# Kernel tuning notes

Hardware: AMD Instinct MI355X
Metric: run time of the kernel (lower is better)

Reference implementation:

```python
import jax, jax.numpy as jnp
import numpy as np

N = 16_777_216  # total nodes
B = 16_384      # graphs per batch


def setup_inputs() -> dict:
    key = jax.random.key(0)
    ks = jax.random.split(key, 9)
    x = jax.random.normal(ks[0], (N, 1), dtype=jnp.float32)
    batch = jnp.sort(jax.random.randint(ks[1], (N,), 0, B)).astype(jnp.int64)
    node_type = jax.random.randint(ks[2], (N,), 0, 3).astype(jnp.int64)
    # MLP params (torch Linear default-ish init scale)
    W1 = jax.random.normal(ks[3], (4, 32), dtype=jnp.float32) * 0.5
    b1 = jax.random.normal(ks[4], (32,), dtype=jnp.float32) * 0.1
    W2 = jax.random.normal(ks[5], (32, 16), dtype=jnp.float32) * 0.18
    b2 = jax.random.normal(ks[6], (16,), dtype=jnp.float32) * 0.1
    W3 = jax.random.normal(ks[7], (16, 1), dtype=jnp.float32) * 0.25
    b3 = jax.random.normal(ks[8], (1,), dtype=jnp.float32) * 0.1
    return {"x": x, "batch": batch, "node_type": node_type, "num_graphs": B,
            "W1": W1, "b1": b1, "W2": W2, "b2": b2, "W3": W3, "b3": b3}


def reference(x, batch, node_type, num_graphs, W1, b1, W2, b2, W3, b3):
    # Per-graph node-type histogram: one fused segment pass over (N, 4)
    # columns = [count(nt==0), count(nt==1), count(nt==2), total_nodes]
    onehot = jax.nn.one_hot(node_type, 3, dtype=jnp.float32)           # (N, 3)
    per_node = jnp.concatenate([onehot, jnp.ones((onehot.shape[0], 1), jnp.float32)], axis=1)  # (N, 4)
    feats = jax.ops.segment_sum(per_node, batch, num_segments=num_graphs)  # (B, 4)
    feats = feats - jnp.array([54.5, 0.0, 0.0, 56.5], dtype=jnp.float32)
    h = jax.nn.relu(feats @ W1 + b1)
    h = jax.nn.relu(h @ W2 + b2)
    return h @ W3 + b3  # (B, 1)
```

## Files before the change

kernel.cpp:

```cpp
#include <hip/hip_runtime.h>


constexpr int GPW = 4;

__device__ __forceinline__ int interp_lower_bound(
    const int* __restrict__ batch, int n, int stride, int g)
{
    int blo = 0, bhi = n;
    long long pos = (long long)g * stride - (stride >> 1);
    int it = 0;
    while (bhi - blo > 4) {
        int p;
        if (it < 5) {
            long long pc = pos;
            if (pc < blo) pc = blo;
            if (pc > bhi - 4) pc = bhi - 4;
            p = (int)pc & ~3;
            ++it;
        } else {
            p = ((blo + bhi) >> 1) & ~3;
            if (p > bhi - 4) p = bhi - 4;
        }
        const int4 q = *(const int4*)(batch + p);
        if (q.w < g) {
            blo = p + 4;
            pos = p + 4 + (long long)(g - q.w) * stride - (stride >> 1);
        } else if (q.x >= g) {
            bhi = p;
            pos = p + (long long)(g - q.x) * stride - (stride >> 1);
        } else {
            return p + 1 + (q.y < g) + (q.z < g);
        }
    }
    if (bhi > blo) {
        const int4 q = *(const int4*)(batch + blo);
        return blo + (q.x < g) + (q.y < g) + (q.z < g) + (q.w < g);
    }
    return blo;
}

__global__ __launch_bounds__(256) void fused_kernel(
    const int* __restrict__ batch, const int* __restrict__ ntype,
    const float* __restrict__ W1, const float* __restrict__ b1,
    const float* __restrict__ W2, const float* __restrict__ b2,
    const float* __restrict__ W3, const float* __restrict__ b3,
    float* __restrict__ out, int n, int B, int stride)
{
    __shared__ float sW1[128], sW2[512], sb1[32], sb2[16], sW3[16], sb3v[1];
    const int tid = threadIdx.x;
    if (tid < 128) sW1[tid] = W1[tid];
    sW2[tid]       = W2[tid];
    sW2[tid + 256] = W2[tid + 256];
    if      (tid < 32)  sb1[tid]      = b1[tid];
    else if (tid < 48)  sb2[tid - 32] = b2[tid - 32];
    else if (tid < 64)  sW3[tid - 48] = W3[tid - 48];
    else if (tid == 64) sb3v[0]       = b3[0];
    __syncthreads();

    const int wid  = (blockIdx.x * 256 + tid) >> 6;
    const int lane = tid & 63;
    const int g0   = wid * GPW;
    if (g0 >= B) return;

    int ans = 0;
    if (lane <= GPW) {
        const int g = min(g0 + lane, B);
        ans = interp_lower_bound(batch, n, stride, g);
    }

    for (int i = 0; i < GPW; ++i) {
        const int g = g0 + i;
        if (g >= B) break;
        const int s   = __shfl(ans, i);
        const int e   = __shfl(ans, i + 1);
        const int len = e - s;

        int c0 = 0, c1 = 0;
        int sa = (s + 3) & ~3; if (sa > e) sa = e;
        int ea = e & ~3;       if (ea < sa) ea = sa;

        {
            const int idx = s + lane;
            if (idx < sa) { const int v = ntype[idx]; c0 += (v == 0); c1 += (v == 1); }
        }
        {
            const int4* nt4 = (const int4*)ntype;
            for (int q = (sa >> 2) + lane; q < (ea >> 2); q += 64) {
                const int4 v = nt4[q];
                c0 += (v.x == 0) + (v.y == 0) + (v.z == 0) + (v.w == 0);
                c1 += (v.x == 1) + (v.y == 1) + (v.z == 1) + (v.w == 1);
            }
        }
        {
            const int idx = ea + lane;
            if (idx < e) { const int v = ntype[idx]; c0 += (v == 0); c1 += (v == 1); }
        }

        unsigned long long p = (unsigned)c0 | ((unsigned long long)(unsigned)c1 << 32);
        #pragma unroll
        for (int off = 32; off; off >>= 1) p += __shfl_xor(p, off);
        const int c0t = (int)(p & 0xFFFFFFFFull);
        const int c1t = (int)(p >> 32);

        const float f0 = (float)c0t - 54.5f;
        const float f1 = (float)c1t;
        const float f2 = (float)(len - c0t - c1t);
        const float f3 = (float)len - 56.5f;

        const int j = lane & 31;
        float h1 = sb1[j];
        h1 = fmaf(f0, sW1[      j], h1);
        h1 = fmaf(f1, sW1[ 32 + j], h1);
        h1 = fmaf(f2, sW1[ 64 + j], h1);
        h1 = fmaf(f3, sW1[ 96 + j], h1);
        h1 = fmaxf(0.0f, h1);

        const int m = lane & 15;
        float s2 = sb2[m];
        #pragma unroll
        for (int jj = 0; jj < 32; ++jj)
            s2 = fmaf(__shfl(h1, jj), sW2[jj * 16 + m], s2);
        const float h2 = fmaxf(0.0f, s2);

        float p3 = h2 * sW3[m];
        p3 += __shfl_xor(p3, 8);
        p3 += __shfl_xor(p3, 4);
        p3 += __shfl_xor(p3, 2);
        p3 += __shfl_xor(p3, 1);

        if (lane == 0) out[g] = p3 + sb3v[0];
    }
}

extern "C" void kernel_launch(void* const* d_in, const int* in_sizes, int n_in,
                              void* d_out, int out_size, void* d_ws, size_t ws_size,
                              hipStream_t stream) {
    const int*   batch = (const int*)d_in[1];
    const int*   ntype = (const int*)d_in[2];
    const float* W1    = (const float*)d_in[4];
    const float* b1    = (const float*)d_in[5];
    const float* W2    = (const float*)d_in[6];
    const float* b2    = (const float*)d_in[7];
    const float* W3    = (const float*)d_in[8];
    const float* b3    = (const float*)d_in[9];
    float*       out   = (float*)d_out;

    const int n = in_sizes[1];
    const int B = out_size;

    const int waves  = (B + GPW - 1) / GPW;
    const int blocks = (waves * 64 + 255) / 256;
    fused_kernel<<<blocks, 256, 0, stream>>>(
        batch, ntype, W1, b1, W2, b2, W3, b3, out, n, B, n / B);
}
```

Baseline: 28.96 us.

## Process two graphs per wave with unrolled clamped loads and split MLP halves

Each wave now handles two graphs instead of four, which doubles the wave count. The streaming loop over node types is unrolled five times with clamped unconditional loads so that many independent 16-byte loads are in flight before the predicated accumulation. The two graphs' reductions are interleaved, and the MLP runs once with each half-wave evaluating one graph, instead of running serially per graph. This targets memory latency and serial per-graph overhead, at the cost of more binary searches overall and some wasted loads on short segments.

```diff
diff --git a/kernel.cpp b/kernel.cpp
--- a/kernel.cpp
+++ b/kernel.cpp
@@ -1,7 +1,8 @@
 #include <hip/hip_runtime.h>
 
 
-constexpr int GPW = 4;
+constexpr int GPW = 2;
+constexpr int UNR = 5;
 
 __device__ __forceinline__ int interp_lower_bound(
     const int* __restrict__ batch, int n, int stride, int g)
@@ -63,73 +64,90 @@
     if (g0 >= B) return;
 
     int ans = 0;
-    if (lane <= GPW) {
-        const int g = min(g0 + lane, B);
-        ans = interp_lower_bound(batch, n, stride, g);
-    }
+    if (lane <= GPW) ans = interp_lower_bound(batch, n, stride, min(g0 + lane, B));
+    const int s0 = __shfl(ans, 0);
+    const int s1 = __shfl(ans, 1);
+    const int s2b = __shfl(ans, 2);
 
-    for (int i = 0; i < GPW; ++i) {
-        const int g = g0 + i;
-        if (g >= B) break;
-        const int s   = __shfl(ans, i);
-        const int e   = __shfl(ans, i + 1);
-        const int len = e - s;
+    const int4* nt4 = (const int4*)ntype;
+    const int nqm1 = (n >> 2) - 1;
+    int c0[2] = {0, 0}, c1[2] = {0, 0};
 
-        int c0 = 0, c1 = 0;
+    #pragma unroll
+    for (int i = 0; i < 2; ++i) {
+        const int s = (i == 0) ? s0 : s1;
+        const int e = (i == 0) ? s1 : s2b;
         int sa = (s + 3) & ~3; if (sa > e) sa = e;
         int ea = e & ~3;       if (ea < sa) ea = sa;
 
         {
             const int idx = s + lane;
-            if (idx < sa) { const int v = ntype[idx]; c0 += (v == 0); c1 += (v == 1); }
+            if (idx < sa) { const int v = ntype[idx]; c0[i] += (v == 0); c1[i] += (v == 1); }
         }
-        {
-            const int4* nt4 = (const int4*)ntype;
-            for (int q = (sa >> 2) + lane; q < (ea >> 2); q += 64) {
-                const int4 v = nt4[q];
-                c0 += (v.x == 0) + (v.y == 0) + (v.z == 0) + (v.w == 0);
-                c1 += (v.x == 1) + (v.y == 1) + (v.z == 1) + (v.w == 1);
+        const int qa = (sa >> 2) + lane;
+        const int qe = (ea >> 2);
+        #pragma unroll
+        for (int u = 0; u < UNR; ++u) {
+            const int qi = qa + u * 64;
+            const int4 v = nt4[min(qi, nqm1)];
+            if (qi < qe) {
+                c0[i] += (v.x == 0) + (v.y == 0) + (v.z == 0) + (v.w == 0);
+                c1[i] += (v.x == 1) + (v.y == 1) + (v.z == 1) + (v.w == 1);
             }
+        }
+        for (int qi = qa + UNR * 64; qi < qe; qi += 64) {
+            const int4 v = nt4[qi];
+            c0[i] += (v.x == 0) + (v.y == 0) + (v.z == 0) + (v.w == 0);
+            c1[i] += (v.x == 1) + (v.y == 1) + (v.z == 1) + (v.w == 1);
         }
         {
             const int idx = ea + lane;
-            if (idx < e) { const int v = ntype[idx]; c0 += (v == 0); c1 += (v == 1); }
+            if (idx < e) { const int v = ntype[idx]; c0[i] += (v == 0); c1[i] += (v == 1); }
         }
+    }
 
-        unsigned long long p = (unsigned)c0 | ((unsigned long long)(unsigned)c1 << 32);
-        #pragma unroll
-        for (int off = 32; off; off >>= 1) p += __shfl_xor(p, off);
-        const int c0t = (int)(p & 0xFFFFFFFFull);
-        const int c1t = (int)(p >> 32);
+    unsigned long long pa = (unsigned)c0[0] | ((unsigned long long)(unsigned)c1[0] << 32);
+    unsigned long long pb = (unsigned)c0[1] | ((unsigned long long)(unsigned)c1[1] << 32);
+    #pragma unroll
+    for (int off = 32; off; off >>= 1) {
+        pa += __shfl_xor(pa, off);
+        pb += __shfl_xor(pb, off);
+    }
 
-        const float f0 = (float)c0t - 54.5f;
-        const float f1 = (float)c1t;
-        const float f2 = (float)(len - c0t - c1t);
-        const float f3 = (float)len - 56.5f;
+    const bool hb = (lane >= 32);
+    const int c0t = hb ? (int)(pb & 0xFFFFFFFFull) : (int)(pa & 0xFFFFFFFFull);
+    const int c1t = hb ? (int)(pb >> 32)           : (int)(pa >> 32);
+    const int len = hb ? (s2b - s1)                : (s1 - s0);
 
-        const int j = lane & 31;
-        float h1 = sb1[j];
-        h1 = fmaf(f0, sW1[      j], h1);
-        h1 = fmaf(f1, sW1[ 32 + j], h1);
-        h1 = fmaf(f2, sW1[ 64 + j], h1);
-        h1 = fmaf(f3, sW1[ 96 + j], h1);
-        h1 = fmaxf(0.0f, h1);
+    const float f0 = (float)c0t - 54.5f;
+    const float f1 = (float)c1t;
+    const float f2 = (float)(len - c0t - c1t);
+    const float f3 = (float)len - 56.5f;
 
-        const int m = lane & 15;
-        float s2 = sb2[m];
-        #pragma unroll
-        for (int jj = 0; jj < 32; ++jj)
-            s2 = fmaf(__shfl(h1, jj), sW2[jj * 16 + m], s2);
-        const float h2 = fmaxf(0.0f, s2);
+    const int j = lane & 31;
+    float h1 = sb1[j];
+    h1 = fmaf(f0, sW1[      j], h1);
+    h1 = fmaf(f1, sW1[ 32 + j], h1);
+    h1 = fmaf(f2, sW1[ 64 + j], h1);
+    h1 = fmaf(f3, sW1[ 96 + j], h1);
+    h1 = fmaxf(0.0f, h1);
 
-        float p3 = h2 * sW3[m];
-        p3 += __shfl_xor(p3, 8);
-        p3 += __shfl_xor(p3, 4);
-        p3 += __shfl_xor(p3, 2);
-        p3 += __shfl_xor(p3, 1);
+    const int m = lane & 15;
+    const int hbase = lane & 32;
+    float sm = sb2[m];
+    #pragma unroll
+    for (int jj = 0; jj < 32; ++jj)
+        sm = fmaf(__shfl(h1, hbase + jj), sW2[jj * 16 + m], sm);
+    const float h2 = fmaxf(0.0f, sm);
 
-        if (lane == 0) out[g] = p3 + sb3v[0];
-    }
+    float p3 = h2 * sW3[m];
+    p3 += __shfl_xor(p3, 8);
+    p3 += __shfl_xor(p3, 4);
+    p3 += __shfl_xor(p3, 2);
+    p3 += __shfl_xor(p3, 1);
+
+    if (lane == 0)                          out[g0]     = p3 + sb3v[0];
+    if (lane == 32 && g0 + 1 < B)           out[g0 + 1] = p3 + sb3v[0];
 }
 
 extern "C" void kernel_launch(void* const* d_in, const int* in_sizes, int n_in,
```

After: 27.26 us. 1.06x faster.

## Assign one graph per wave with unrolled clamped loads and split MLP layer

Applied to the files above, without the earlier changes.

Each wave now handles a single graph instead of four, so there are four times as many waves. The int4 counting loop is unrolled five deep, using clamped addresses so all loads can be issued before the predicated accumulation. The second MLP layer is split across the two half-waves, each summing 16 inputs, and the halves are combined with one xor shuffle. This shortens the dependent chains and exposes more memory-level parallelism, at the cost of more waves and more boundary searches per wave.

```diff
diff --git a/kernel.cpp b/kernel.cpp
--- a/kernel.cpp
+++ b/kernel.cpp
@@ -1,7 +1,7 @@
 #include <hip/hip_runtime.h>
 
 
-constexpr int GPW = 4;
+constexpr int UNR = 5;
 
 __device__ __forceinline__ int interp_lower_bound(
     const int* __restrict__ batch, int n, int stride, int g)
@@ -57,79 +57,83 @@
     else if (tid == 64) sb3v[0]       = b3[0];
     __syncthreads();
 
-    const int wid  = (blockIdx.x * 256 + tid) >> 6;
+    const int g    = (blockIdx.x * 256 + tid) >> 6;
     const int lane = tid & 63;
-    const int g0   = wid * GPW;
-    if (g0 >= B) return;
+    if (g >= B) return;
 
     int ans = 0;
-    if (lane <= GPW) {
-        const int g = min(g0 + lane, B);
-        ans = interp_lower_bound(batch, n, stride, g);
+    if (lane <= 1) ans = interp_lower_bound(batch, n, stride, g + lane);
+    const int s = __shfl(ans, 0);
+    const int e = __shfl(ans, 1);
+    const int len = e - s;
+
+    const int4* nt4 = (const int4*)ntype;
+    const int nqm1 = (n >> 2) - 1;
+    int c0 = 0, c1 = 0;
+
+    int sa = (s + 3) & ~3; if (sa > e) sa = e;
+    int ea = e & ~3;       if (ea < sa) ea = sa;
+
+    {
+        const int idx = s + lane;
+        if (idx < sa) { const int v = ntype[idx]; c0 += (v == 0); c1 += (v == 1); }
+    }
+    const int qa = (sa >> 2) + lane;
+    const int qe = (ea >> 2);
+    #pragma unroll
+    for (int u = 0; u < UNR; ++u) {
+        const int qi = qa + u * 64;
+        const int4 v = nt4[min(qi, nqm1)];
+        if (qi < qe) {
+            c0 += (v.x == 0) + (v.y == 0) + (v.z == 0) + (v.w == 0);
+            c1 += (v.x == 1) + (v.y == 1) + (v.z == 1) + (v.w == 1);
+        }
+    }
+    for (int qi = qa + UNR * 64; qi < qe; qi += 64) {
+        const int4 v = nt4[qi];
+        c0 += (v.x == 0) + (v.y == 0) + (v.z == 0) + (v.w == 0);
+        c1 += (v.x == 1) + (v.y == 1) + (v.z == 1) + (v.w == 1);
+    }
+    {
+        const int idx = ea + lane;
+        if (idx < e) { const int v = ntype[idx]; c0 += (v == 0); c1 += (v == 1); }
     }
 
-    for (int i = 0; i < GPW; ++i) {
-        const int g = g0 + i;
-        if (g >= B) break;
-        const int s   = __shfl(ans, i);
-        const int e   = __shfl(ans, i + 1);
-        const int len = e - s;
+    unsigned long long p = (unsigned)c0 | ((unsigned long long)(unsigned)c1 << 32);
+    #pragma unroll
+    for (int off = 32; off; off >>= 1) p += __shfl_xor(p, off);
+    const int c0t = (int)(p & 0xFFFFFFFFull);
+    const int c1t = (int)(p >> 32);
 
-        int c0 = 0, c1 = 0;
-        int sa = (s + 3) & ~3; if (sa > e) sa = e;
-        int ea = e & ~3;       if (ea < sa) ea = sa;
+    const float f0 = (float)c0t - 54.5f;
+    const float f1 = (float)c1t;
+    const float f2 = (float)(len - c0t - c1t);
+    const float f3 = (float)len - 56.5f;
 
-        {
-            const int idx = s + lane;
-            if (idx < sa) { const int v = ntype[idx]; c0 += (v == 0); c1 += (v == 1); }
-        }
-        {
-            const int4* nt4 = (const int4*)ntype;
-            for (int q = (sa >> 2) + lane; q < (ea >> 2); q += 64) {
-                const int4 v = nt4[q];
-                c0 += (v.x == 0) + (v.y == 0) + (v.z == 0) + (v.w == 0);
-                c1 += (v.x == 1) + (v.y == 1) + (v.z == 1) + (v.w == 1);
-            }
-        }
-        {
-            const int idx = ea + lane;
-            if (idx < e) { const int v = ntype[idx]; c0 += (v == 0); c1 += (v == 1); }
-        }
+    const int j = lane & 31;
+    float h1 = sb1[j];
+    h1 = fmaf(f0, sW1[      j], h1);
+    h1 = fmaf(f1, sW1[ 32 + j], h1);
+    h1 = fmaf(f2, sW1[ 64 + j], h1);
+    h1 = fmaf(f3, sW1[ 96 + j], h1);
+    h1 = fmaxf(0.0f, h1);
 
-        unsigned long long p = (unsigned)c0 | ((unsigned long long)(unsigned)c1 << 32);
-        #pragma unroll
-        for (int off = 32; off; off >>= 1) p += __shfl_xor(p, off);
-        const int c0t = (int)(p & 0xFFFFFFFFull);
-        const int c1t = (int)(p >> 32);
+    const int m = lane & 15;
+    const int jb = lane & 16;
+    float sm = 0.0f;
+    #pragma unroll
+    for (int jj = 0; jj < 16; ++jj)
+        sm = fmaf(__shfl(h1, jb + jj), sW2[(jb + jj) * 16 + m], sm);
+    sm += __shfl_xor(sm, 16);
+    const float h2 = fmaxf(0.0f, sm + sb2[m]);
 
-        const float f0 = (float)c0t - 54.5f;
-        const float f1 = (float)c1t;
-        const float f2 = (float)(len - c0t - c1t);
-        const float f3 = (float)len - 56.5f;
+    float p3 = h2 * sW3[m];
+    p3 += __shfl_xor(p3, 8);
+    p3 += __shfl_xor(p3, 4);
+    p3 += __shfl_xor(p3, 2);
+    p3 += __shfl_xor(p3, 1);
 
-        const int j = lane & 31;
-        float h1 = sb1[j];
-        h1 = fmaf(f0, sW1[      j], h1);
-        h1 = fmaf(f1, sW1[ 32 + j], h1);
-        h1 = fmaf(f2, sW1[ 64 + j], h1);
-        h1 = fmaf(f3, sW1[ 96 + j], h1);
-        h1 = fmaxf(0.0f, h1);
-
-        const int m = lane & 15;
-        float s2 = sb2[m];
-        #pragma unroll
-        for (int jj = 0; jj < 32; ++jj)
-            s2 = fmaf(__shfl(h1, jj), sW2[jj * 16 + m], s2);
-        const float h2 = fmaxf(0.0f, s2);
-
-        float p3 = h2 * sW3[m];
-        p3 += __shfl_xor(p3, 8);
-        p3 += __shfl_xor(p3, 4);
-        p3 += __shfl_xor(p3, 2);
-        p3 += __shfl_xor(p3, 1);
-
-        if (lane == 0) out[g] = p3 + sb3v[0];
-    }
+    if (lane == 0) out[g] = p3 + sb3v[0];
 }
 
 extern "C" void kernel_launch(void* const* d_in, const int* in_sizes, int n_in,
@@ -148,8 +152,7 @@
     const int n = in_sizes[1];
     const int B = out_size;
 
-    const int waves  = (B + GPW - 1) / GPW;
-    const int blocks = (waves * 64 + 255) / 256;
+    const int blocks = (B * 64 + 255) / 256;
     fused_kernel<<<blocks, 256, 0, stream>>>(
         batch, ntype, W1, b1, W2, b2, W3, b3, out, n, B, n / B);
 }
```

New measurement: 33.64 us. 1.16x slower.
